# Performance work log

Hardware: AMD Instinct MI355X
Metric: run time of the kernel (lower is better)

Reference implementation:

```python
import jax, jax.numpy as jnp
import numpy as np
from math import factorial, sqrt

# static config matching cg_interaction(l1=3, l2=3, l_middel=2, l_out=3, channel=128)
L1 = 3; L2 = 3; MIDDLE = 2; LOUT = 3; CHANNEL = 128; EDGES = 65536
DIM1 = (L1 + 1) ** 2  # 16
DIM2 = (L2 + 1) ** 2  # 16


def _su2_cg(j1, m1, j2, m2, j3, m3):
    # standard Clebsch-Gordan coefficient <j1 m1 j2 m2 | j3 m3> (Racah formula)
    if m3 != m1 + m2:
        return 0.0
    f = factorial
    pref = sqrt((2 * j3 + 1) * f(j3 + j1 - j2) * f(j3 - j1 + j2) * f(j1 + j2 - j3) / f(j1 + j2 + j3 + 1))
    pref *= sqrt(f(j3 + m3) * f(j3 - m3) * f(j1 - m1) * f(j1 + m1) * f(j2 - m2) * f(j2 + m2))
    kmin = max(0, j2 - j3 - m1, j1 - j3 + m2)
    kmax = min(j1 + j2 - j3, j1 - m1, j2 + m2)
    s = 0.0
    for k in range(kmin, kmax + 1):
        s += (-1) ** k / (f(k) * f(j1 + j2 - j3 - k) * f(j1 - m1 - k) * f(j2 + m2 - k) * f(j3 - j2 + m1 + k) * f(j3 - j1 - m2 + k))
    return pref * s


def _q_real_to_complex(l):
    # e3nn change-of-basis real->complex spherical harmonics
    q = np.zeros((2 * l + 1, 2 * l + 1), dtype=np.complex128)
    for m in range(-l, 0):
        q[l + m, l + abs(m)] = 1 / sqrt(2)
        q[l + m, l - abs(m)] = -1j / sqrt(2)
    q[l, l] = 1.0
    for m in range(1, l + 1):
        q[l + m, l + abs(m)] = (-1) ** m / sqrt(2)
        q[l + m, l - abs(m)] = 1j * (-1) ** m / sqrt(2)
    return (-1j) ** l * q


def _w3j(l1, l2, l3):
    # real Wigner-3j tensor, unit Frobenius norm (e3nn convention up to global sign)
    C = np.zeros((2 * l1 + 1, 2 * l2 + 1, 2 * l3 + 1))
    for m1 in range(-l1, l1 + 1):
        for m2 in range(-l2, l2 + 1):
            m3 = m1 + m2
            if abs(m3) <= l3:
                C[l1 + m1, l2 + m2, l3 + m3] = _su2_cg(l1, m1, l2, m2, l3, m3)
    Q1, Q2, Q3 = _q_real_to_complex(l1), _q_real_to_complex(l2), _q_real_to_complex(l3)
    Cr = np.einsum('ij,kl,nm,ikm->jln', Q1, Q2, np.conj(Q3), C.astype(np.complex128))
    Cr = np.real(Cr)
    return (Cr / np.linalg.norm(Cr)).astype(np.float32)


# output irrep entries (mul, l): [scalars(0e), gate-scalars(0e), gated l=1.., ...]
ENTRIES_CG = [(CHANNEL, 0), (CHANNEL * MIDDLE, 0)] + [(CHANNEL, l) for l in range(1, MIDDLE + 1)]
ENTRIES_ALL = [(1, 0), (LOUT, 0)] + [(1, l) for l in range(1, LOUT + 1)]


def _paths(entries):
    p = []
    for ei, (mul, lo) in enumerate(entries):
        for la in range(L1 + 1):
            for lb in range(L2 + 1):
                if (la + lb + lo) % 2 == 0 and abs(la - lb) <= lo <= la + lb:
                    p.append((la, lb, ei))
    return p


PATHS_CG = _paths(ENTRIES_CG)
PATHS_ALL = _paths(ENTRIES_ALL)
NW_CG = sum(ENTRIES_CG[ei][0] for _, _, ei in PATHS_CG)   # 3200
NW_ALL = sum(ENTRIES_ALL[ei][0] for _, _, ei in PATHS_ALL)  # 35
NB_CG = sum(m for m, l in ENTRIES_CG if l == 0)  # 384
NB_ALL = sum(m for m, l in ENTRIES_ALL if l == 0)  # 4

_keys = set()
for la, lb, ei in PATHS_CG:
    _keys.add((la, lb, ENTRIES_CG[ei][1]))
for la, lb, ei in PATHS_ALL:
    _keys.add((la, lb, ENTRIES_ALL[ei][1]))
W3J = {k: jnp.asarray(_w3j(*k)) for k in sorted(_keys)}


def _tp(x, y, w, b, entries, paths):
    # fully-connected tensor product (mul-1 inputs) with per-output-entry
    # sqrt((2l+1)/num_paths) normalization and bias on 0e entries
    blocks = [None] * len(entries)
    npaths = [0] * len(entries)
    for _, _, ei in paths:
        npaths[ei] += 1
    off = 0
    for la, lb, ei in paths:
        mul, lo = entries[ei]
        xs = x[:, la * la:(la + 1) * (la + 1)]
        ys = y[:, lb * lb:(lb + 1) * (lb + 1)]
        z = jnp.einsum('ei,ej,ijk->ek', xs, ys, W3J[(la, lb, lo)])  # (E, 2lo+1)
        c = z[:, None, :] * w[off:off + mul][None, :, None]         # (E, mul, 2lo+1)
        blocks[ei] = c if blocks[ei] is None else blocks[ei] + c
        off += mul
    boff = 0
    outs = []
    for ei, (mul, lo) in enumerate(entries):
        blk = blocks[ei] * np.float32(sqrt((2 * lo + 1) / max(npaths[ei], 1)))
        if lo == 0:
            blk = blk + b[boff:boff + mul][None, :, None]
            boff += mul
        outs.append(blk)
    return outs


def _forward(x, y, w_cg, b_cg, w_all, b_all):
    # --- cg branch: channelled mid-degree TP + SwishGate + degree reshape ---
    outs = _tp(x, y, w_cg, b_cg, ENTRIES_CG, PATHS_CG)
    sc = jax.nn.silu(outs[0][..., 0])                    # (E, C)
    gates = jax.nn.sigmoid(outs[1][..., 0])              # (E, C*MIDDLE)
    rows = [sc[:, None, :]]                              # degree-0 row of reshape output
    for l in range(1, MIDDLE + 1):
        g = gates[:, (l - 1) * CHANNEL:l * CHANNEL]      # (E, C)
        gated = outs[1 + l] * g[:, :, None]              # (E, C, 2l+1)
        rows.append(jnp.transpose(gated, (0, 2, 1)))     # (E, 2l+1, C)
    cg_low = jnp.concatenate(rows, axis=1)               # (E, (MIDDLE+1)^2, C)
    # --- cg_all branch: mul-1 TP up to l_out + SwishGate ---
    outs_a = _tp(x, y, w_all, b_all, ENTRIES_ALL, PATHS_ALL)
    pieces = [jax.nn.silu(outs_a[0][..., 0])]            # (E, 1)
    ga = jax.nn.sigmoid(outs_a[1][..., 0])               # (E, LOUT)
    for l in range(1, LOUT + 1):
        pieces.append(outs_a[1 + l][:, 0, :] * ga[:, l - 1:l])  # (E, 2l+1)
    cg_all = jnp.concatenate(pieces, axis=1)             # (E, (LOUT+1)^2)
    return cg_low, cg_all


def setup_inputs() -> dict:
    key = jax.random.key(0)
    k1, k2, k3, k4, k5, k6 = jax.random.split(key, 6)
    x = jax.random.normal(k1, (EDGES, DIM1), jnp.float32)
    y = jax.random.normal(k2, (EDGES, DIM2), jnp.float32)
    w_cg = jax.random.normal(k3, (NW_CG,), jnp.float32) * 0.3
    b_cg = jax.random.normal(k4, (NB_CG,), jnp.float32) * 0.1
    w_all = jax.random.normal(k5, (NW_ALL,), jnp.float32) * 0.3
    b_all = jax.random.normal(k6, (NB_ALL,), jnp.float32) * 0.1
    return {"x": x, "y": y, "w_cg": w_cg, "b_cg": b_cg, "w_all": w_all, "b_all": b_all}


def reference(x, y, w_cg, b_cg, w_all, b_all):
    return _forward(x, y, w_cg, b_cg, w_all, b_all)
```

## Files before the change

### kernel.cpp

```cpp
#include <hip/hip_runtime.h>
#include <utility>

namespace w3j_gen {

struct FactT { double f[16]; };
constexpr FactT make_fact() {
    FactT t{}; t.f[0] = 1.0;
    for (int i = 1; i < 16; i++) t.f[i] = t.f[i-1] * (double)i;
    return t;
}
constexpr FactT FT = make_fact();

constexpr double csqrt(double x) {
    if (x <= 0.0) return 0.0;
    double g = x < 1.0 ? 1.0 : x;
    for (int i = 0; i < 80; i++) g = 0.5 * (g + x / g);
    return g;
}

constexpr int imax3(int a, int b, int c) { int m = a; if (b > m) m = b; if (c > m) m = c; return m; }
constexpr int imin3(int a, int b, int c) { int m = a; if (b < m) m = b; if (c < m) m = c; return m; }

constexpr double su2_cg(int j1, int m1, int j2, int m2, int j3, int m3) {
    if (m3 != m1 + m2) return 0.0;
    double pref = csqrt((double)(2*j3+1) * FT.f[j3+j1-j2] * FT.f[j3-j1+j2] * FT.f[j1+j2-j3] / FT.f[j1+j2+j3+1]);
    pref *= csqrt(FT.f[j3+m3] * FT.f[j3-m3] * FT.f[j1-m1] * FT.f[j1+m1] * FT.f[j2-m2] * FT.f[j2+m2]);
    int kmin = imax3(0, j2-j3-m1, j1-j3+m2);
    int kmax = imin3(j1+j2-j3, j1-m1, j2+m2);
    double s = 0.0;
    for (int k = kmin; k <= kmax; k++) {
        double d = FT.f[k] * FT.f[j1+j2-j3-k] * FT.f[j1-m1-k] * FT.f[j2+m2-k] * FT.f[j3-j2+m1+k] * FT.f[j3-j1-m2+k];
        s += ((k & 1) ? -1.0 : 1.0) / d;
    }
    return pref * s;
}

struct CD { double re, im; };
struct QT { CD q[7][7]; };

constexpr QT make_q(int l) {
    QT t{};
    const double is2 = csqrt(0.5);
    for (int m = -l; m < 0; m++) {
        t.q[l+m][l-m].re = is2;
        t.q[l+m][l+m].im = -is2;
    }
    t.q[l][l].re = 1.0;
    for (int m = 1; m <= l; m++) {
        double s = (m & 1) ? -1.0 : 1.0;
        t.q[l+m][l+m].re = s * is2;
        t.q[l+m][l-m].im = s * is2;
    }
    CD ph = {1.0, 0.0};
    if (l % 4 == 1) ph = {0.0, -1.0};
    else if (l % 4 == 2) ph = {-1.0, 0.0};
    else if (l % 4 == 3) ph = {0.0, 1.0};
    for (int i = 0; i < 7; i++)
        for (int j = 0; j < 7; j++) {
            CD a = t.q[i][j];
            t.q[i][j] = { ph.re*a.re - ph.im*a.im, ph.re*a.im + ph.im*a.re };
        }
    return t;
}

struct Tab { float v[245]; };

constexpr Tab make_w3j(int l1, int l2, int l3) {
    const int n1 = 2*l1+1, n2 = 2*l2+1, n3 = 2*l3+1;
    double C[7][7][7] = {};
    for (int m1 = -l1; m1 <= l1; m1++)
        for (int m2 = -l2; m2 <= l2; m2++) {
            int m3 = m1 + m2;
            if (m3 >= -l3 && m3 <= l3)
                C[l1+m1][l2+m2][l3+m3] = su2_cg(l1, m1, l2, m2, l3, m3);
        }
    QT Q1 = make_q(l1), Q2 = make_q(l2), Q3 = make_q(l3);
    CD T1[7][7][7] = {};
    for (int j = 0; j < n1; j++)
        for (int k = 0; k < n2; k++)
            for (int m = 0; m < n3; m++) {
                double sr = 0, si = 0;
                for (int i = 0; i < n1; i++) {
                    double cv = C[i][k][m];
                    sr += Q1.q[i][j].re * cv;
                    si += Q1.q[i][j].im * cv;
                }
                T1[j][k][m] = {sr, si};
            }
    CD T2[7][7][7] = {};
    for (int j = 0; j < n1; j++)
        for (int l = 0; l < n2; l++)
            for (int m = 0; m < n3; m++) {
                double sr = 0, si = 0;
                for (int k = 0; k < n2; k++) {
                    CD a = Q2.q[k][l], b = T1[j][k][m];
                    sr += a.re*b.re - a.im*b.im;
                    si += a.re*b.im + a.im*b.re;
                }
                T2[j][l][m] = {sr, si};
            }
    double Cr[7][7][7] = {};
    double nrm2 = 0.0;
    for (int j = 0; j < n1; j++)
        for (int l = 0; l < n2; l++)
            for (int n = 0; n < n3; n++) {
                double s = 0;
                for (int m = 0; m < n3; m++) {
                    CD a = Q3.q[n][m], b = T2[j][l][m];
                    s += a.re*b.re + a.im*b.im;
                }
                Cr[j][l][n] = s;
                nrm2 += s * s;
            }
    double inv = 1.0 / csqrt(nrm2);
    Tab t{};
    for (int j = 0; j < n1; j++)
        for (int l = 0; l < n2; l++)
            for (int n = 0; n < n3; n++)
                t.v[(j*n2 + l)*n3 + n] = (float)(Cr[j][l][n] * inv);
    return t;
}

constexpr Tab T0  = make_w3j(0,0,0);
constexpr Tab T1_ = make_w3j(1,1,0);
constexpr Tab T2_ = make_w3j(2,2,0);
constexpr Tab T3_ = make_w3j(3,3,0);
constexpr Tab T4  = make_w3j(0,1,1);
constexpr Tab T5  = make_w3j(1,0,1);
constexpr Tab T6  = make_w3j(1,2,1);
constexpr Tab T7  = make_w3j(2,1,1);
constexpr Tab T8  = make_w3j(2,3,1);
constexpr Tab T9  = make_w3j(3,2,1);
constexpr Tab T10 = make_w3j(0,2,2);
constexpr Tab T11 = make_w3j(1,1,2);
constexpr Tab T12 = make_w3j(1,3,2);
constexpr Tab T13 = make_w3j(2,0,2);
constexpr Tab T14 = make_w3j(2,2,2);
constexpr Tab T15 = make_w3j(3,1,2);
constexpr Tab T16 = make_w3j(3,3,2);
constexpr Tab T17 = make_w3j(0,3,3);
constexpr Tab T18 = make_w3j(1,2,3);
constexpr Tab T19 = make_w3j(2,1,3);
constexpr Tab T20 = make_w3j(2,3,3);
constexpr Tab T21 = make_w3j(3,0,3);
constexpr Tab T22 = make_w3j(3,2,3);

constexpr int KLA[23]   = {0,1,2,3, 0,1,1,2,2,3, 0,1,1,2,2,3,3, 0,1,2,2,3,3};
constexpr int KLB[23]   = {0,1,2,3, 1,0,2,1,3,2, 2,1,3,0,2,1,3, 3,2,1,3,0,2};
constexpr int KLO[23]   = {0,0,0,0, 1,1,1,1,1,1, 2,2,2,2,2,2,2, 3,3,3,3,3,3};
constexpr int KZOFF[23] = {0,1,2,3, 4,7,10,13,16,19, 22,27,32,37,42,47,52, 57,64,71,78,85,92};

struct Term { int i, j, k; float w; };
struct TermList { Term t[1875]; int koff[24]; int n; };

constexpr TermList build_terms() {
    TermList L{};
    const Tab* ts[23] = {&T0,&T1_,&T2_,&T3_,&T4,&T5,&T6,&T7,&T8,&T9,&T10,&T11,
                         &T12,&T13,&T14,&T15,&T16,&T17,&T18,&T19,&T20,&T21,&T22};
    for (int key = 0; key < 23; key++) {
        L.koff[key] = L.n;
        const int la = KLA[key], lb = KLB[key], lo = KLO[key];
        const int n1 = 2*la+1, n2 = 2*lb+1, n3 = 2*lo+1;
        for (int i = 0; i < n1; i++)
            for (int j = 0; j < n2; j++)
                for (int k = 0; k < n3; k++) {
                    float w = ts[key]->v[(i*n2+j)*n3+k];
                    float aw = w < 0 ? -w : w;
                    if (aw > 1e-6f) {
                        L.t[L.n].i = la*la + i;
                        L.t[L.n].j = lb*lb + j;
                        L.t[L.n].k = KZOFF[key] + k;
                        L.t[L.n].w = w;
                        L.n++;
                    }
                }
    }
    L.koff[23] = L.n;
    return L;
}
constexpr TermList TL = build_terms();

constexpr int find_split(int target) {
    for (int k = 0; k <= 23; k++) if (TL.koff[k] >= target) return k;
    return 23;
}
constexpr int S1 = find_split(TL.n / 4);
constexpr int S2 = find_split(TL.n / 2);
constexpr int S3 = find_split(3 * TL.n / 4);

}

template <int KEY, size_t... I>
__device__ __forceinline__ void term_unroll(float* __restrict__ acc,
                                            const float* __restrict__ xv,
                                            const float* __restrict__ yv,
                                            std::index_sequence<I...>) {
    constexpr int t0 = w3j_gen::TL.koff[KEY];
    ((acc[w3j_gen::TL.t[t0 + I].k - w3j_gen::KZOFF[KEY]] +=
          w3j_gen::TL.t[t0 + I].w * xv[w3j_gen::TL.t[t0 + I].i] * yv[w3j_gen::TL.t[t0 + I].j]), ...);
}

template <int KEY>
__device__ __forceinline__ void key_accum(float* __restrict__ zrow,
                                          const float* __restrict__ xv,
                                          const float* __restrict__ yv) {
    constexpr int n3 = 2 * w3j_gen::KLO[KEY] + 1;
    constexpr int nt = w3j_gen::TL.koff[KEY + 1] - w3j_gen::TL.koff[KEY];
    float acc[n3] = {};
    term_unroll<KEY>(acc, xv, yv, std::make_index_sequence<(size_t)nt>{});
    #pragma unroll
    for (int k = 0; k < n3; k++) zrow[w3j_gen::KZOFF[KEY] + k] = acc[k];
}

template <int FROM, size_t... K>
__device__ __forceinline__ void keys_range(float* __restrict__ zrow,
                                           const float* __restrict__ xv,
                                           const float* __restrict__ yv,
                                           std::index_sequence<K...>) {
    (key_accum<FROM + (int)K>(zrow, xv, yv), ...);
}

#define N_EDGES   65536
#define TILE      64
#define ZROW      108
#define ALL_BASE  75497472ull

typedef float f32x4 __attribute__((ext_vector_type(4)));

__device__ __forceinline__ float sigmoidf_(float v) { return 1.0f / (1.0f + __expf(-v)); }

__global__ __launch_bounds__(256, 2)
void cg_interaction_kernel(
    const float* __restrict__ x, const float* __restrict__ y,
    const float* __restrict__ w_cg, const float* __restrict__ b_cg,
    const float* __restrict__ w_all, const float* __restrict__ b_all,
    float* __restrict__ out)
{
    __shared__ __align__(16) float zs[TILE][ZROW];

    const int tid = threadIdx.x;
    const int e0 = blockIdx.x * TILE;

    {
        const int eidx = tid & 63;
        const int esub = tid >> 6;
        float xv[16], yv[16];
        const float4* xp = (const float4*)(x + (size_t)(e0 + eidx) * 16);
        const float4* yp = (const float4*)(y + (size_t)(e0 + eidx) * 16);
        #pragma unroll
        for (int q = 0; q < 4; q++) {
            float4 v = xp[q];
            xv[4*q+0] = v.x; xv[4*q+1] = v.y; xv[4*q+2] = v.z; xv[4*q+3] = v.w;
            float4 u = yp[q];
            yv[4*q+0] = u.x; yv[4*q+1] = u.y; yv[4*q+2] = u.z; yv[4*q+3] = u.w;
        }
        using namespace w3j_gen;
        float* zrow = &zs[eidx][0];
        if (esub == 0)      keys_range<0 >(zrow, xv, yv, std::make_index_sequence<S1>{});
        else if (esub == 1) keys_range<S1>(zrow, xv, yv, std::make_index_sequence<S2 - S1>{});
        else if (esub == 2) keys_range<S2>(zrow, xv, yv, std::make_index_sequence<S3 - S2>{});
        else                keys_range<S3>(zrow, xv, yv, std::make_index_sequence<23 - S3>{});
    }
    __syncthreads();

    const int cq = (tid & 31) << 2;
    const int es = tid >> 5;

    float w00[4][4], wg1[4][4], wg2[4][4];
    #pragma unroll
    for (int p = 0; p < 4; p++) {
        float4 a = *(const float4*)(w_cg + p * 128 + cq);
        w00[p][0]=a.x; w00[p][1]=a.y; w00[p][2]=a.z; w00[p][3]=a.w;
        float4 b = *(const float4*)(w_cg + 512 + p * 256 + cq);
        wg1[p][0]=b.x; wg1[p][1]=b.y; wg1[p][2]=b.z; wg1[p][3]=b.w;
        float4 d = *(const float4*)(w_cg + 640 + p * 256 + cq);
        wg2[p][0]=d.x; wg2[p][1]=d.y; wg2[p][2]=d.z; wg2[p][3]=d.w;
    }
    float wl1[6][4];
    #pragma unroll
    for (int p = 0; p < 6; p++) {
        float4 a = *(const float4*)(w_cg + 1536 + p * 128 + cq);
        wl1[p][0]=a.x; wl1[p][1]=a.y; wl1[p][2]=a.z; wl1[p][3]=a.w;
    }
    float wl2[7][4];
    #pragma unroll
    for (int p = 0; p < 7; p++) {
        float4 a = *(const float4*)(w_cg + 2304 + p * 128 + cq);
        wl2[p][0]=a.x; wl2[p][1]=a.y; wl2[p][2]=a.z; wl2[p][3]=a.w;
    }
    float b0[4], b1[4], b2[4];
    {
        float4 a = *(const float4*)(b_cg + cq);
        b0[0]=a.x; b0[1]=a.y; b0[2]=a.z; b0[3]=a.w;
        float4 b = *(const float4*)(b_cg + 128 + cq);
        b1[0]=b.x; b1[1]=b.y; b1[2]=b.z; b1[3]=b.w;
        float4 d = *(const float4*)(b_cg + 256 + cq);
        b2[0]=d.x; b2[1]=d.y; b2[2]=d.z; b2[3]=d.w;
    }

    const float SQ12 = 0.70710678118654752f;
    const float SQ57 = 0.84515425472851657f;

    float* o = out + (size_t)(e0 + es) * 1152 + cq;
    for (int t = es; t < TILE; t += 8, o += 8 * 1152) {
        const float* zrow = &zs[t][0];
        float zz[60];
        #pragma unroll
        for (int q = 0; q < 15; q++) {
            float4 v = *(const float4*)(zrow + 4 * q);
            zz[4*q+0] = v.x; zz[4*q+1] = v.y; zz[4*q+2] = v.z; zz[4*q+3] = v.w;
        }

        float sc[4], g1[4], g2[4];
        #pragma unroll
        for (int j = 0; j < 4; j++) {
            float u0 = (zz[0]*w00[0][j] + zz[1]*w00[1][j] + zz[2]*w00[2][j] + zz[3]*w00[3][j]) * 0.5f + b0[j];
            float u1 = (zz[0]*wg1[0][j] + zz[1]*wg1[1][j] + zz[2]*wg1[2][j] + zz[3]*wg1[3][j]) * 0.5f + b1[j];
            float u2 = (zz[0]*wg2[0][j] + zz[1]*wg2[1][j] + zz[2]*wg2[2][j] + zz[3]*wg2[3][j]) * 0.5f + b2[j];
            sc[j] = u0 * sigmoidf_(u0);
            g1[j] = sigmoidf_(u1) * SQ12;
            g2[j] = sigmoidf_(u2) * SQ57;
        }

        f32x4 r0 = { sc[0], sc[1], sc[2], sc[3] };
        __builtin_nontemporal_store(r0, (f32x4*)o);
        #pragma unroll
        for (int k = 0; k < 3; k++) {
            float s[4];
            #pragma unroll
            for (int j = 0; j < 4; j++) {
                float a = 0.0f;
                #pragma unroll
                for (int p = 0; p < 6; p++) a += zz[4 + 3*p + k] * wl1[p][j];
                s[j] = a * g1[j];
            }
            f32x4 r = { s[0], s[1], s[2], s[3] };
            __builtin_nontemporal_store(r, (f32x4*)(o + (1 + k) * 128));
        }
        #pragma unroll
        for (int k = 0; k < 5; k++) {
            float s[4];
            #pragma unroll
            for (int j = 0; j < 4; j++) {
                float a = 0.0f;
                #pragma unroll
                for (int p = 0; p < 7; p++) a += zz[22 + 5*p + k] * wl2[p][j];
                s[j] = a * g2[j];
            }
            f32x4 r = { s[0], s[1], s[2], s[3] };
            __builtin_nontemporal_store(r, (f32x4*)(o + (4 + k) * 128));
        }
    }

    if (tid < 128) {
        const int c = tid & 15;
        const int es2 = tid >> 4;
        const float SQ76 = 1.08012344973464f;

        if (c == 0) {
            const float gw0 = w_all[0], gw1 = w_all[1], gw2 = w_all[2], gw3 = w_all[3], gb = b_all[0];
            for (int t = es2; t < TILE; t += 8) {
                const float* zr = &zs[t][0];
                float g = (zr[0]*gw0 + zr[1]*gw1 + zr[2]*gw2 + zr[3]*gw3) * 0.5f + gb;
                __builtin_nontemporal_store(g * sigmoidf_(g), out + ALL_BASE + (size_t)(e0 + t) * 16);
            }
        } else if (c < 4) {
            const float gw0 = w_all[4], gw1 = w_all[7], gw2 = w_all[10], gw3 = w_all[13], gb = b_all[1];
            float aw[6];
            #pragma unroll
            for (int p = 0; p < 6; p++) aw[p] = w_all[16 + p];
            const int zb = 4 + (c - 1);
            for (int t = es2; t < TILE; t += 8) {
                const float* zr = &zs[t][0];
                float g = (zr[0]*gw0 + zr[1]*gw1 + zr[2]*gw2 + zr[3]*gw3) * 0.5f + gb;
                float s = 0.0f;
                #pragma unroll
                for (int p = 0; p < 6; p++) s += aw[p] * zr[zb + 3*p];
                __builtin_nontemporal_store(s * SQ12 * sigmoidf_(g),
                                            out + ALL_BASE + (size_t)(e0 + t) * 16 + c);
            }
        } else if (c < 9) {
            const float gw0 = w_all[5], gw1 = w_all[8], gw2 = w_all[11], gw3 = w_all[14], gb = b_all[2];
            float aw[7];
            #pragma unroll
            for (int p = 0; p < 7; p++) aw[p] = w_all[22 + p];
            const int zb = 22 + (c - 4);
            for (int t = es2; t < TILE; t += 8) {
                const float* zr = &zs[t][0];
                float g = (zr[0]*gw0 + zr[1]*gw1 + zr[2]*gw2 + zr[3]*gw3) * 0.5f + gb;
                float s = 0.0f;
                #pragma unroll
                for (int p = 0; p < 7; p++) s += aw[p] * zr[zb + 5*p];
                __builtin_nontemporal_store(s * SQ57 * sigmoidf_(g),
                                            out + ALL_BASE + (size_t)(e0 + t) * 16 + c);
            }
        } else {
            const float gw0 = w_all[6], gw1 = w_all[9], gw2 = w_all[12], gw3 = w_all[15], gb = b_all[3];
            float aw[6];
            #pragma unroll
            for (int p = 0; p < 6; p++) aw[p] = w_all[29 + p];
            const int zb = 57 + (c - 9);
            for (int t = es2; t < TILE; t += 8) {
                const float* zr = &zs[t][0];
                float g = (zr[0]*gw0 + zr[1]*gw1 + zr[2]*gw2 + zr[3]*gw3) * 0.5f + gb;
                float s = 0.0f;
                #pragma unroll
                for (int p = 0; p < 6; p++) s += aw[p] * zr[zb + 7*p];
                __builtin_nontemporal_store(s * SQ76 * sigmoidf_(g),
                                            out + ALL_BASE + (size_t)(e0 + t) * 16 + c);
            }
        }
    }
}

extern "C" void kernel_launch(void* const* d_in, const int* in_sizes, int n_in,
                              void* d_out, int out_size, void* d_ws, size_t ws_size,
                              hipStream_t stream) {
    const float* x     = (const float*)d_in[0];
    const float* y     = (const float*)d_in[1];
    const float* w_cg  = (const float*)d_in[2];
    const float* b_cg  = (const float*)d_in[3];
    const float* w_all = (const float*)d_in[4];
    const float* b_all = (const float*)d_in[5];
    float* out = (float*)d_out;

    dim3 grid(N_EDGES / TILE), block(256);
    hipLaunchKernelGGL(cg_interaction_kernel, grid, block, 0, stream,
                       x, y, w_cg, b_cg, w_all, b_all, out);
}
```

Before: 333.4 us.

## Halve edge tile, split CG terms eight ways, stage z loads to cut registers

Shrinks the per-block edge tile from 64 to 32 so the CG phase now splits the term list across eight thread groups instead of four. It raises the launch-bounds occupancy hint from 2 to 3 blocks per SM. It also replaces the single 60-float load of the shared z row with staged loads for the l=0, l=1 and l=2 segments, lowering peak register pressure. The aim is more resident waves and better latency hiding on a store-bound kernel, at the cost of twice as many blocks and repeated weight loads per block.

```diff
diff --git a/kernel.cpp b/kernel.cpp
--- a/kernel.cpp
+++ b/kernel.cpp
@@ -184,9 +184,11 @@
     for (int k = 0; k <= 23; k++) if (TL.koff[k] >= target) return k;
     return 23;
 }
-constexpr int S1 = find_split(TL.n / 4);
-constexpr int S2 = find_split(TL.n / 2);
-constexpr int S3 = find_split(3 * TL.n / 4);
+constexpr int SP[9] = {0,
+    find_split(TL.n * 1 / 8), find_split(TL.n * 2 / 8),
+    find_split(TL.n * 3 / 8), find_split(TL.n * 4 / 8),
+    find_split(TL.n * 5 / 8), find_split(TL.n * 6 / 8),
+    find_split(TL.n * 7 / 8), 23};
 
 }
 
@@ -221,7 +223,7 @@
 }
 
 #define N_EDGES   65536
-#define TILE      64
+#define TILE      32
 #define ZROW      108
 #define ALL_BASE  75497472ull
 
@@ -229,7 +231,7 @@
 
 __device__ __forceinline__ float sigmoidf_(float v) { return 1.0f / (1.0f + __expf(-v)); }
 
-__global__ __launch_bounds__(256, 2)
+__global__ __launch_bounds__(256, 3)
 void cg_interaction_kernel(
     const float* __restrict__ x, const float* __restrict__ y,
     const float* __restrict__ w_cg, const float* __restrict__ b_cg,
@@ -242,8 +244,8 @@
     const int e0 = blockIdx.x * TILE;
 
     {
-        const int eidx = tid & 63;
-        const int esub = tid >> 6;
+        const int eidx = tid & 31;
+        const int esub = tid >> 5;
         float xv[16], yv[16];
         const float4* xp = (const float4*)(x + (size_t)(e0 + eidx) * 16);
         const float4* yp = (const float4*)(y + (size_t)(e0 + eidx) * 16);
@@ -256,10 +258,16 @@
         }
         using namespace w3j_gen;
         float* zrow = &zs[eidx][0];
-        if (esub == 0)      keys_range<0 >(zrow, xv, yv, std::make_index_sequence<S1>{});
-        else if (esub == 1) keys_range<S1>(zrow, xv, yv, std::make_index_sequence<S2 - S1>{});
-        else if (esub == 2) keys_range<S2>(zrow, xv, yv, std::make_index_sequence<S3 - S2>{});
-        else                keys_range<S3>(zrow, xv, yv, std::make_index_sequence<23 - S3>{});
+        switch (esub) {
+        case 0: keys_range<SP[0]>(zrow, xv, yv, std::make_index_sequence<SP[1]-SP[0]>{}); break;
+        case 1: keys_range<SP[1]>(zrow, xv, yv, std::make_index_sequence<SP[2]-SP[1]>{}); break;
+        case 2: keys_range<SP[2]>(zrow, xv, yv, std::make_index_sequence<SP[3]-SP[2]>{}); break;
+        case 3: keys_range<SP[3]>(zrow, xv, yv, std::make_index_sequence<SP[4]-SP[3]>{}); break;
+        case 4: keys_range<SP[4]>(zrow, xv, yv, std::make_index_sequence<SP[5]-SP[4]>{}); break;
+        case 5: keys_range<SP[5]>(zrow, xv, yv, std::make_index_sequence<SP[6]-SP[5]>{}); break;
+        case 6: keys_range<SP[6]>(zrow, xv, yv, std::make_index_sequence<SP[7]-SP[6]>{}); break;
+        default: keys_range<SP[7]>(zrow, xv, yv, std::make_index_sequence<SP[8]-SP[7]>{}); break;
+        }
     }
     __syncthreads();
 
@@ -304,26 +312,27 @@
     float* o = out + (size_t)(e0 + es) * 1152 + cq;
     for (int t = es; t < TILE; t += 8, o += 8 * 1152) {
         const float* zrow = &zs[t][0];
-        float zz[60];
-        #pragma unroll
-        for (int q = 0; q < 15; q++) {
-            float4 v = *(const float4*)(zrow + 4 * q);
-            zz[4*q+0] = v.x; zz[4*q+1] = v.y; zz[4*q+2] = v.z; zz[4*q+3] = v.w;
-        }
-
+
+        float4 z03 = *(const float4*)zrow;
         float sc[4], g1[4], g2[4];
         #pragma unroll
         for (int j = 0; j < 4; j++) {
-            float u0 = (zz[0]*w00[0][j] + zz[1]*w00[1][j] + zz[2]*w00[2][j] + zz[3]*w00[3][j]) * 0.5f + b0[j];
-            float u1 = (zz[0]*wg1[0][j] + zz[1]*wg1[1][j] + zz[2]*wg1[2][j] + zz[3]*wg1[3][j]) * 0.5f + b1[j];
-            float u2 = (zz[0]*wg2[0][j] + zz[1]*wg2[1][j] + zz[2]*wg2[2][j] + zz[3]*wg2[3][j]) * 0.5f + b2[j];
+            float u0 = (z03.x*w00[0][j] + z03.y*w00[1][j] + z03.z*w00[2][j] + z03.w*w00[3][j]) * 0.5f + b0[j];
+            float u1 = (z03.x*wg1[0][j] + z03.y*wg1[1][j] + z03.z*wg1[2][j] + z03.w*wg1[3][j]) * 0.5f + b1[j];
+            float u2 = (z03.x*wg2[0][j] + z03.y*wg2[1][j] + z03.z*wg2[2][j] + z03.w*wg2[3][j]) * 0.5f + b2[j];
             sc[j] = u0 * sigmoidf_(u0);
             g1[j] = sigmoidf_(u1) * SQ12;
             g2[j] = sigmoidf_(u2) * SQ57;
         }
-
         f32x4 r0 = { sc[0], sc[1], sc[2], sc[3] };
         __builtin_nontemporal_store(r0, (f32x4*)o);
+
+        float zl[20];
+        #pragma unroll
+        for (int q = 0; q < 5; q++) {
+            float4 v = *(const float4*)(zrow + 4 + 4 * q);
+            zl[4*q+0] = v.x; zl[4*q+1] = v.y; zl[4*q+2] = v.z; zl[4*q+3] = v.w;
+        }
         #pragma unroll
         for (int k = 0; k < 3; k++) {
             float s[4];
@@ -331,12 +340,21 @@
             for (int j = 0; j < 4; j++) {
                 float a = 0.0f;
                 #pragma unroll
-                for (int p = 0; p < 6; p++) a += zz[4 + 3*p + k] * wl1[p][j];
+                for (int p = 0; p < 6; p++) a += zl[3*p + k] * wl1[p][j];
                 s[j] = a * g1[j];
             }
             f32x4 r = { s[0], s[1], s[2], s[3] };
             __builtin_nontemporal_store(r, (f32x4*)(o + (1 + k) * 128));
         }
+
+        float zh[35];
+        zh[0] = zl[18]; zh[1] = zl[19];
+        #pragma unroll
+        for (int q = 0; q < 8; q++) {
+            float4 v = *(const float4*)(zrow + 24 + 4 * q);
+            zh[2+4*q+0] = v.x; zh[2+4*q+1] = v.y; zh[2+4*q+2] = v.z; zh[2+4*q+3] = v.w;
+        }
+        zh[34] = zrow[56];
         #pragma unroll
         for (int k = 0; k < 5; k++) {
             float s[4];
@@ -344,7 +362,7 @@
             for (int j = 0; j < 4; j++) {
                 float a = 0.0f;
                 #pragma unroll
-                for (int p = 0; p < 7; p++) a += zz[22 + 5*p + k] * wl2[p][j];
+                for (int p = 0; p < 7; p++) a += zh[5*p + k] * wl2[p][j];
                 s[j] = a * g2[j];
             }
             f32x4 r = { s[0], s[1], s[2], s[3] };
```

Result: no change. 330.5 us (-0.9%).
